# Kernel tuning notes

Measured on AMD Instinct MI355X. Metric: run time of the kernel, lower is better.

The kernel has to match this reference:

```python
import jax, jax.numpy as jnp
import numpy as np

MOLS = 64
ATOMS = 256
N = MOLS * ATOMS
K_GB = 32
K_GNN = 16
HID = 128
OFFSET = 0.009            # GB dielectric offset (nm)
ALPHA, BETA, GAMMA = 1.0, 0.8, 4.85  # OBC2 coefficients
EPS_FACTOR = 138.935456   # Coulomb constant, kJ*nm/(mol*e^2)
PREF = -EPS_FACTOR * (1.0 - 1.0 / 78.5)


def _edges(key, k_neigh):
    # random intra-molecule neighbors, no self loops (mimics radius-graph structure)
    src = jnp.repeat(jnp.arange(N), k_neigh)
    off = jax.random.randint(key, (N * k_neigh,), 1, ATOMS)
    dst = (src // ATOMS) * ATOMS + (src % ATOMS + off) % ATOMS
    return jnp.stack([src, dst]).astype(jnp.int32)


def setup_inputs() -> dict:
    key = jax.random.key(0)
    ks = jax.random.split(key, 8)
    pos = (jax.random.uniform(ks[0], (N, 3), jnp.float32) * 1.5)
    q = jax.random.uniform(ks[1], (N, 1), jnp.float32) - 0.5
    rad = 0.15 + 0.05 * jax.random.uniform(ks[2], (N, 1), jnp.float32)
    scl = 0.8 + 0.2 * jax.random.uniform(ks[3], (N, 1), jnp.float32)
    rest = jax.random.uniform(ks[4], (N, 4), jnp.float32)
    atom_features = jnp.concatenate([q, rad, scl, rest], axis=1)
    batch = jnp.repeat(jnp.arange(MOLS), ATOMS).astype(jnp.int32)
    edge_index = _edges(ks[5], K_GB)
    gnn_edge_index = _edges(ks[6], K_GNN)

    def lin(k, fi, fo):
        return (jax.random.normal(k, (fi, fo), jnp.float32) / np.float32(np.sqrt(fi)),
                jnp.zeros((fo,), jnp.float32))
    kw = jax.random.split(ks[7], 6)
    i1_w1, i1_b1 = lin(kw[0], 2 * 2 + 1, HID)
    i1_w2, i1_b2 = lin(kw[1], HID, HID)
    i2_w1, i2_b1 = lin(kw[2], 2 * HID + 1, HID)
    i2_w2, i2_b2 = lin(kw[3], HID, HID)
    i3_w1, i3_b1 = lin(kw[4], 2 * HID + 1, HID)
    i3_w2, i3_b2 = lin(kw[5], HID, 1)
    return dict(pos=pos, atom_features=atom_features, batch=batch,
                edge_index=edge_index, gnn_edge_index=gnn_edge_index,
                i1_w1=i1_w1, i1_b1=i1_b1, i1_w2=i1_w2, i1_b2=i1_b2,
                i2_w1=i2_w1, i2_b1=i2_b1, i2_w2=i2_w2, i2_b2=i2_b2,
                i3_w1=i3_w1, i3_b1=i3_b1, i3_w2=i3_w2, i3_b2=i3_b2)


def _dist(pos, ei):
    d2 = jnp.sum((pos[ei[0]] - pos[ei[1]]) ** 2, axis=1)
    return jnp.sqrt(d2 + 1e-12)


def _gb_energies(pos, feats, ei):
    # GBNeck_interaction (Born radii via HCT descreening integral, OBC2 rescale)
    # followed by GBNeck_energies (pairwise GB + self energy), per-atom [N,1]
    n = pos.shape[0]
    src, dst = ei[0], ei[1]
    d = _dist(pos, ei)
    q, radius, scale = feats[:, 0], feats[:, 1], feats[:, 2]
    rho = radius - OFFSET
    sr_j = (scale * rho)[src]
    rho_i = rho[dst]
    U = d + sr_j
    L = jnp.maximum(rho_i, jnp.abs(d - sr_j))
    I = 0.5 * (1.0 / L - 1.0 / U
               + 0.25 * (d - sr_j ** 2 / d) * (1.0 / U ** 2 - 1.0 / L ** 2)
               + 0.5 * jnp.log(L / U) / d)
    I = jnp.where(rho_i < U, I, 0.0)
    Isum = jax.ops.segment_sum(I, dst, num_segments=n)
    psi = Isum * rho
    B = 1.0 / (1.0 / rho - jnp.tanh(ALPHA * psi - BETA * psi ** 2 + GAMMA * psi ** 3) / radius)
    Bi, Bj = B[dst], B[src]
    f_gb = jnp.sqrt(d ** 2 + Bi * Bj * jnp.exp(-d ** 2 / (4.0 * Bi * Bj)))
    e_pair = 0.5 * PREF * q[dst] * q[src] / f_gb  # 0.5: edges are double counted
    e = 0.5 * PREF * q ** 2 / B + jax.ops.segment_sum(e_pair, dst, num_segments=n)
    return e[:, None]


def _in_layer(x, ei, d, w1, b1, w2, b2):
    # IN_layer_all_swish_2pass: edge MLP on [x_i || x_j || d] + scatter-add
    n = x.shape[0]
    m = jnp.concatenate([x[ei[0]], x[ei[1]], d[:, None]], axis=1)
    h = jax.nn.silu(m @ w1 + b1)
    return jax.ops.segment_sum(h @ w2 + b2, ei[1], num_segments=n)


def _energies_all(pos, feats, ei, gei,
                  i1_w1, i1_b1, i1_w2, i1_b2,
                  i2_w1, i2_b1, i2_w2, i2_b2,
                  i3_w1, i3_b1, i3_w2, i3_b2):
    e_gb = _gb_energies(pos, feats, ei)
    d_gnn = _dist(pos, gei)
    x = jax.nn.silu(_in_layer(feats[:, :2], gei, d_gnn, i1_w1, i1_b1, i1_w2, i1_b2))
    x = jax.nn.silu(_in_layer(x, gei, d_gnn, i2_w1, i2_b1, i2_w2, i2_b2))
    x = _in_layer(x, gei, d_gnn, i3_w1, i3_b1, i3_w2, i3_b2)
    return e_gb + x


def reference(pos, atom_features, batch, edge_index, gnn_edge_index,
              i1_w1, i1_b1, i1_w2, i1_b2,
              i2_w1, i2_b1, i2_w2, i2_b2,
              i3_w1, i3_b1, i3_w2, i3_b2):
    ws = (i1_w1, i1_b1, i1_w2, i1_b2, i2_w1, i2_b1, i2_w2, i2_b2,
          i3_w1, i3_b1, i3_w2, i3_b2)
    efun = lambda p: _energies_all(p, atom_features, edge_index, gnn_edge_index, *ws)
    energies, vjp = jax.vjp(efun, pos)  # [N,1]
    (gpos,) = vjp(jnp.ones_like(energies))
    forces = -gpos
    energy = jax.ops.segment_sum(energies[:, 0], batch, num_segments=MOLS)[:, None]
    return energy, forces
```

## Files before the change

kernel.cpp:

```cpp
#include <hip/hip_runtime.h>
#include <hip/hip_bf16.h>

#define NATOMS 16384
#define MOLS   64
#define ATOMSM 256
#define EGB    524288
#define EGNN   262144
#define HID    128
#define NH     (NATOMS*HID)

#define OFFSETC 0.009f
#define ALPHAC  1.0f
#define BETAC   0.8f
#define GAMMAC  4.85f
#define PREFC   (-138.935456f*(1.0f-1.0f/78.5f))

typedef __hip_bfloat16 bf;
typedef __attribute__((ext_vector_type(8))) short bf8v;
typedef __attribute__((ext_vector_type(4))) float f4v;

__device__ __forceinline__ float b2f(bf x){ return __bfloat162float(x); }
__device__ __forceinline__ bf f2b(float x){ return __float2bfloat16(x); }
__device__ __forceinline__ short f2s(float x){ bf h = f2b(x); return *(short*)&h; }
__device__ __forceinline__ float s2f(short s){
    unsigned int x = ((unsigned int)(unsigned short)s) << 16;
    return __uint_as_float(x);
}
__device__ __forceinline__ float sigf(float x){ return 1.0f/(1.0f+__expf(-x)); }
__device__ __forceinline__ float waveRed(float v){
    v += __shfl_xor(v,32); v += __shfl_xor(v,16); v += __shfl_xor(v,8);
    v += __shfl_xor(v,4);  v += __shfl_xor(v,2);  v += __shfl_xor(v,1);
    return v;
}

__global__ __launch_bounds__(256) void k_gbA_dist(
    const float* __restrict__ pos, const float* __restrict__ feat,
    const int* __restrict__ ei, float* __restrict__ Isum,
    const int* __restrict__ gei, float* __restrict__ dgnn, int* __restrict__ cnt)
{
    int tid = threadIdx.x;
    if (blockIdx.x < 512){
        __shared__ float sPx[256], sPy[256], sPz[256], sRho[256], sSr[256];
        __shared__ float sI[256];
        int mbase = (blockIdx.x >> 3) * 256;
        {
            int i = mbase + tid;
            sPx[tid]=pos[3*i]; sPy[tid]=pos[3*i+1]; sPz[tid]=pos[3*i+2];
            float rad = feat[7*i+1], sc = feat[7*i+2];
            float rho = rad - OFFSETC;
            sRho[tid]=rho; sSr[tid]=sc*rho;
            sI[tid]=0.f;
        }
        __syncthreads();
        int T = blockIdx.x*256 + tid;
        int s = T >> 3, p = T & 7;
        int sl = s & 255;
        int e0 = s*32 + p*4;
        float px = sPx[sl], py = sPy[sl], pz = sPz[sl];
        float sr = sSr[sl];
        const int* dP = ei + EGB;
#pragma unroll
        for (int j=0;j<4;j++){
            int dl = dP[e0+j] & 255;
            float dx = px - sPx[dl];
            float dy = py - sPy[dl];
            float dz = pz - sPz[dl];
            float d  = sqrtf(dx*dx+dy*dy+dz*dz + 1e-12f);
            float rho_i = sRho[dl];
            float U = d + sr;
            if (rho_i < U){
                float L = fmaxf(rho_i, fabsf(d - sr));
                float invU = 1.0f/U, invL = 1.0f/L;
                float I = 0.5f*invL - 0.5f*invU
                        + 0.125f*(d - sr*sr/d)*(invU*invU - invL*invL)
                        + 0.25f*__logf(L*invU)/d;
                atomicAdd(&sI[dl], I);
            }
        }
        __syncthreads();
        atomicAdd(&Isum[mbase + tid], sI[tid]);
    } else {
        int e = (blockIdx.x-512)*256 + tid;
        if (e >= EGNN) return;
        int s = gei[e], dd = gei[EGNN+e];
        float dx = pos[3*s+0] - pos[3*dd+0];
        float dy = pos[3*s+1] - pos[3*dd+1];
        float dz = pos[3*s+2] - pos[3*dd+2];
        dgnn[e] = sqrtf(dx*dx+dy*dy+dz*dz + 1e-12f);
        atomicAdd(&cnt[dd], 1);
    }
}

__global__ __launch_bounds__(256) void k_gbB_scan(
    const float* __restrict__ feat, const float* __restrict__ Isum,
    float* __restrict__ Bv, float* __restrict__ cB, float* __restrict__ gB,
    float* __restrict__ egb,
    const int* __restrict__ cnt, int* __restrict__ rptr, int* __restrict__ cursor)
{
    int t = threadIdx.x;
    if (blockIdx.x < 64){
        int i = blockIdx.x*256 + t;
        float q   = feat[7*i+0];
        float rad = feat[7*i+1];
        float rho = rad - OFFSETC;
        float psi = Isum[i]*rho;
        float u = psi*(ALPHAC + psi*(-BETAC + GAMMAC*psi));
        float tt = tanhf(u);
        float B = 1.0f/(1.0f/rho - tt/rad);
        Bv[i] = B;
        float du = ALPHAC + psi*(-2.0f*BETAC + 3.0f*GAMMAC*psi);
        cB[i] = B*B*((1.0f-tt*tt)/rad)*du*rho;
        float Cs = 0.5f*PREFC*q*q;
        egb[i] = Cs/B;
        gB[i]  = -Cs/(B*B);
    } else {
        __shared__ int sc[256];
        int m = blockIdx.x - 64;
        int c = cnt[m*256+t];
        sc[t] = c; __syncthreads();
        for (int off=1; off<256; off<<=1){
            int x = (t>=off) ? sc[t-off] : 0;
            __syncthreads();
            sc[t] += x;
            __syncthreads();
        }
        int ex = m*4096 + sc[t] - c;
        rptr[m*256+t] = ex;
        cursor[m*256+t] = ex;
    }
}

__global__ __launch_bounds__(256) void k_gbC(
    const float* __restrict__ pos, const float* __restrict__ feat,
    const int* __restrict__ ei, const float* __restrict__ Bv,
    float* __restrict__ egb, float* __restrict__ gdgb, float* __restrict__ gB)
{
    __shared__ float sPx[256], sPy[256], sPz[256], sB[256], sQf[256];
    __shared__ float sE[256], sG[256];
    int tid = threadIdx.x;
    int mbase = (blockIdx.x >> 3) * 256;
    {
        int i = mbase + tid;
        sPx[tid]=pos[3*i]; sPy[tid]=pos[3*i+1]; sPz[tid]=pos[3*i+2];
        sB[tid]=Bv[i]; sQf[tid]=feat[7*i+0];
        sE[tid]=0.f; sG[tid]=0.f;
    }
    __syncthreads();
    int T = blockIdx.x*256 + tid;
    int s = T >> 3, p = T & 7;
    int sl = s & 255;
    int e0 = s*32 + p*4;
    float px = sPx[sl], py = sPy[sl], pz = sPz[sl];
    float qs = sQf[sl];
    float Bs = sB[sl];
    float gsrc = 0.f;
    const int* dP = ei + EGB;
#pragma unroll
    for (int j=0;j<4;j++){
        int dl = dP[e0+j] & 255;
        float dx = px - sPx[dl];
        float dy = py - sPy[dl];
        float dz = pz - sPz[dl];
        float d2 = dx*dx+dy*dy+dz*dz + 1e-12f;
        float d  = sqrtf(d2);
        float Bd = sB[dl];
        float C = 0.5f*PREFC*sQf[dl]*qs;
        float P = Bd*Bs;
        float ex = __expf(-d2/(4.f*P));
        float f2 = d2 + P*ex;
        float f  = sqrtf(f2);
        float f3i = 1.f/(f2*f);
        gdgb[e0+j] = -C*d*(1.f - 0.25f*ex)*f3i;
        float common = -C*ex*(1.f + d2/(4.f*P))*0.5f*f3i;
        atomicAdd(&sE[dl], C/f);
        atomicAdd(&sG[dl], common*Bs);
        gsrc += common*Bd;
    }
    gsrc += __shfl_xor(gsrc,1);
    gsrc += __shfl_xor(gsrc,2);
    gsrc += __shfl_xor(gsrc,4);
    if (p==0) atomicAdd(&sG[sl], gsrc);
    __syncthreads();
    atomicAdd(&egb[mbase + tid], sE[tid]);
    atomicAdd(&gB[mbase + tid],  sG[tid]);
}

__global__ __launch_bounds__(256) void k_gbE(
    const float* __restrict__ pos, const float* __restrict__ feat,
    const int* __restrict__ ei, const float* __restrict__ cB,
    const float* __restrict__ gB,
    const float* __restrict__ gdgb, float* __restrict__ grad)
{
    __shared__ float sPx[256], sPy[256], sPz[256], sRho[256], sSr[256], sCg[256];
    __shared__ float sGx[256], sGy[256], sGz[256];
    int tid = threadIdx.x;
    int mbase = (blockIdx.x >> 3) * 256;
    {
        int i = mbase + tid;
        sPx[tid]=pos[3*i]; sPy[tid]=pos[3*i+1]; sPz[tid]=pos[3*i+2];
        float rad = feat[7*i+1], sc = feat[7*i+2];
        float rho = rad - OFFSETC;
        sRho[tid]=rho; sSr[tid]=sc*rho;
        sCg[tid]=cB[i]*gB[i];
        sGx[tid]=0.f; sGy[tid]=0.f; sGz[tid]=0.f;
    }
    __syncthreads();
    int T = blockIdx.x*256 + tid;
    int s = T >> 3, p = T & 7;
    int sl = s & 255;
    int e0 = s*32 + p*4;
    float px = sPx[sl], py = sPy[sl], pz = sPz[sl];
    float sr = sSr[sl];
    float gx=0.f, gy=0.f, gz=0.f;
    const int* dP = ei + EGB;
#pragma unroll
    for (int j=0;j<4;j++){
        int dl = dP[e0+j] & 255;
        float dx = px - sPx[dl];
        float dy = py - sPy[dl];
        float dz = pz - sPz[dl];
        float d2 = dx*dx+dy*dy+dz*dz + 1e-12f;
        float d  = sqrtf(d2);
        float rho_i = sRho[dl];
        float U = d + sr;
        float gd = gdgb[e0+j];
        if (rho_i < U){
            float aa = fabsf(d - sr);
            float L, Lp;
            if (rho_i >= aa){ L = rho_i; Lp = 0.f; }
            else { L = aa; Lp = (d >= sr) ? 1.f : -1.f; }
            float invU = 1.f/U, invL = 1.f/L;
            float invU2=invU*invU, invL2=invL*invL;
            float dIdd = -0.5f*Lp*invL2 + 0.5f*invU2
                + 0.125f*(1.f + sr*sr/d2)*(invU2 - invL2)
                + 0.125f*(d - sr*sr/d)*(2.f*Lp*invL2*invL - 2.f*invU2*invU)
                + 0.25f*((Lp*invL - invU)/d - __logf(L*invU)/d2);
            gd += sCg[dl]*dIdd;
        }
        float c = gd/d;
        gx += c*dx; gy += c*dy; gz += c*dz;
        atomicAdd(&sGx[dl], -c*dx);
        atomicAdd(&sGy[dl], -c*dy);
        atomicAdd(&sGz[dl], -c*dz);
    }
    gx += __shfl_xor(gx,1); gx += __shfl_xor(gx,2); gx += __shfl_xor(gx,4);
    gy += __shfl_xor(gy,1); gy += __shfl_xor(gy,2); gy += __shfl_xor(gy,4);
    gz += __shfl_xor(gz,1); gz += __shfl_xor(gz,2); gz += __shfl_xor(gz,4);
    if (p==0){
        atomicAdd(&sGx[sl], gx);
        atomicAdd(&sGy[sl], gy);
        atomicAdd(&sGz[sl], gz);
    }
    __syncthreads();
    int i = mbase + tid;
    atomicAdd(&grad[3*i+0], sGx[tid]);
    atomicAdd(&grad[3*i+1], sGy[tid]);
    atomicAdd(&grad[3*i+2], sGz[tid]);
}

__global__ __launch_bounds__(256) void k_fill(
    const int* __restrict__ gei, int* __restrict__ cursor, int* __restrict__ csr)
{
    int e = blockIdx.x*256 + threadIdx.x;
    if (e >= EGNN) return;
    int dst = gei[EGNN+e];
    int pos = atomicAdd(&cursor[dst], 1);
    csr[pos] = e;
}

__global__ __launch_bounds__(256) void k_pre(
    const float* __restrict__ A2, const float* __restrict__ C1,
    const float* __restrict__ A3, const float* __restrict__ C2,
    short* __restrict__ C1t, short* __restrict__ C2t,
    short* __restrict__ A2at, short* __restrict__ A2bt,
    short* __restrict__ A3at, short* __restrict__ A3bt,
    short* __restrict__ rA2a, short* __restrict__ rA2b,
    short* __restrict__ rA3a, short* __restrict__ rA3b,
    short* __restrict__ rC1, short* __restrict__ rC2,
    const float* __restrict__ feat, const float* __restrict__ A1,
    bf* __restrict__ u1, bf* __restrict__ v1)
{
    if (blockIdx.x < 64){
        int gid = blockIdx.x*256 + threadIdx.x;
        int j = gid >> 7, k = gid & 127;
        C1t[gid]  = f2s(C1[k*HID+j]);
        C2t[gid]  = f2s(C2[k*HID+j]);
        A2at[gid] = f2s(A2[k*HID+j]);
        A2bt[gid] = f2s(A2[(HID+k)*HID+j]);
        A3at[gid] = f2s(A3[k*HID+j]);
        A3bt[gid] = f2s(A3[(HID+k)*HID+j]);
        rA2a[gid] = f2s(A2[gid]);
        rA2b[gid] = f2s(A2[HID*HID+gid]);
        rA3a[gid] = f2s(A3[gid]);
        rA3b[gid] = f2s(A3[HID*HID+gid]);
        rC1[gid]  = f2s(C1[gid]);
        rC2[gid]  = f2s(C2[gid]);
    } else {
        int gid = (blockIdx.x-64)*256 + threadIdx.x;
        int i = gid >> 7, k = gid & 127;
        float q = feat[7*i+0], r = feat[7*i+1];
        u1[gid] = f2b(q*A1[k]       + r*A1[HID+k]);
        v1[gid] = f2b(q*A1[2*HID+k] + r*A1[3*HID+k]);
    }
}

__global__ __launch_bounds__(128) void k_edge_fwd_dst(
    const int* __restrict__ csr, const int* __restrict__ rptr, const int* __restrict__ cnt,
    const float* __restrict__ dgnn, const bf* __restrict__ u, const bf* __restrict__ v,
    const float* __restrict__ wdp, const float* __restrict__ bb,
    bf* __restrict__ Hs, bf* __restrict__ Sds)
{
    int dst = blockIdx.x, k = threadIdx.x;
    int n = cnt[dst], r0 = rptr[dst];
    float wd = wdp[k];
    float base = b2f(v[dst*HID+k]) + bb[k];
    float hsum = 0.f, dssum = 0.f;
    const short* us = (const short*)u;
#pragma unroll 2
    for (int j=0;j<n;j++){
        int e = csr[r0+j];
        float a = s2f(us[(size_t)(e>>4)*HID + k]) + base + dgnn[e]*wd;
        float sg = sigf(a);
        hsum += a*sg;
        dssum += sg*(1.f + a*(1.f - sg));
    }
    Hs[dst*HID+k] = f2b(hsum);
    Sds[dst*HID+k] = f2b(dssum);
}

__global__ __launch_bounds__(256) void k_node_fwd_uv_mfma(
    const short* __restrict__ Hs, const int* __restrict__ cnt,
    const short* __restrict__ Ct, const float* __restrict__ D,
    const short* __restrict__ Aat, const short* __restrict__ Abt,
    bf* __restrict__ dsz, bf* __restrict__ u, bf* __restrict__ v)
{
    __shared__ short sx[64*HID];
    int lane = threadIdx.x & 63, w = threadIdx.x >> 6;
    int m0 = blockIdx.x*64 + w*16;
    int ar = lane & 15, kg = lane >> 4;
    bf8v af[4];
#pragma unroll
    for (int s=0;s<4;s++) af[s] = *(const bf8v*)&Hs[(size_t)(m0+ar)*HID + s*32 + kg*8];
    f4v acc[8];
#pragma unroll
    for (int nt=0;nt<8;nt++){
        acc[nt] = (f4v){0.f,0.f,0.f,0.f};
        const short* bp = Ct + (nt*16+ar)*HID + kg*8;
#pragma unroll
        for (int s=0;s<4;s++){
            bf8v bv = *(const bf8v*)(bp + s*32);
            acc[nt] = __builtin_amdgcn_mfma_f32_16x16x32_bf16(af[s], bv, acc[nt], 0,0,0);
        }
    }
    float cn[4];
#pragma unroll
    for (int r=0;r<4;r++) cn[r] = (float)cnt[m0 + kg*4 + r];
#pragma unroll
    for (int nt=0;nt<8;nt++){
        int j = nt*16 + ar;
        float Dj = D[j];
#pragma unroll
        for (int r=0;r<4;r++){
            int m = m0 + kg*4 + r;
            float zv = acc[nt][r] + cn[r]*Dj;
            float sg = sigf(zv);
// ... 60 lines not shown
#pragma unroll
        for (int s=0;s<4;s++)
            ad_[s] = *(const bf8v*)&Gd[(size_t)(m0+ar)*HID + s*32 + kg*8];
    }
    f4v acc[8];
#pragma unroll
    for (int nt=0;nt<8;nt++){
        acc[nt] = (f4v){0.f,0.f,0.f,0.f};
        const short* bpa = Ra + (nt*16+ar)*HID + kg*8;
        const short* bpb = Rb + (nt*16+ar)*HID + kg*8;
#pragma unroll
        for (int s=0;s<4;s++){
            bf8v ba = *(const bf8v*)(bpa + s*32);
            bf8v bb = *(const bf8v*)(bpb + s*32);
            acc[nt] = __builtin_amdgcn_mfma_f32_16x16x32_bf16(as_[s], ba, acc[nt], 0,0,0);
            acc[nt] = __builtin_amdgcn_mfma_f32_16x16x32_bf16(ad_[s], bb, acc[nt], 0,0,0);
        }
    }
#pragma unroll
    for (int nt=0;nt<8;nt++){
        int j = nt*16 + ar;
#pragma unroll
        for (int r=0;r<4;r++){
            int m = m0 + kg*4 + r;
            float t = acc[nt][r] * b2f(dsz[(size_t)m*HID + j]);
            st[(w*16 + kg*4 + r)*HID + j] = f2s(t);
        }
    }
    __syncthreads();
    bf8v af[4];
#pragma unroll
    for (int s=0;s<4;s++) af[s] = *(const bf8v*)&st[(w*16+ar)*HID + s*32 + kg*8];
    f4v a2[8];
#pragma unroll
    for (int nt=0;nt<8;nt++){
        a2[nt] = (f4v){0.f,0.f,0.f,0.f};
        const short* bp = Rc + (nt*16+ar)*HID + kg*8;
#pragma unroll
        for (int s=0;s<4;s++){
            bf8v bc = *(const bf8v*)(bp + s*32);
            a2[nt] = __builtin_amdgcn_mfma_f32_16x16x32_bf16(af[s], bc, a2[nt], 0,0,0);
        }
    }
#pragma unroll
    for (int nt=0;nt<8;nt++){
        int j = nt*16 + ar;
#pragma unroll
        for (int r=0;r<4;r++){
            gHout[(size_t)(m0 + kg*4 + r)*HID + j] = f2b(a2[nt][r]);
        }
    }
}

__global__ __launch_bounds__(128) void k_l3_dst(
    const int* __restrict__ csr, const int* __restrict__ rptr, const int* __restrict__ cnt,
    const float* __restrict__ dgnn, const bf* __restrict__ u, const bf* __restrict__ v,
    const float* __restrict__ A3, const float* __restrict__ B3,
    const float* __restrict__ C3, const float* __restrict__ D3,
    bf* __restrict__ Gd, float* __restrict__ x3)
{
    __shared__ float rr[2];
    int dst = blockIdx.x, k = threadIdx.x;
    int n = cnt[dst], r0 = rptr[dst];
    float wd = A3[256*HID+k], ck = C3[k];
    float base = b2f(v[dst*HID+k]) + B3[k];
    float hsum = 0.f, dssum = 0.f;
    const short* us = (const short*)u;
#pragma unroll 2
    for (int j=0;j<n;j++){
        int e = csr[r0+j];
        float a = s2f(us[(size_t)(e>>4)*HID + k]) + base + dgnn[e]*wd;
        float sg = sigf(a);
        hsum += a*sg;
        dssum += sg*(1.f + a*(1.f - sg));
    }
    Gd[dst*HID+k] = f2b(ck*dssum);
    float pv = waveRed(ck*hsum);
    if ((k&63)==0) rr[k>>6] = pv;
    __syncthreads();
    if (k==0) x3[dst] = rr[0] + rr[1] + (float)n*D3[0];
}

__global__ __launch_bounds__(128) void k_l3_src(
    const int* __restrict__ gei, const float* __restrict__ dgnn,
    const bf* __restrict__ u, const bf* __restrict__ v,
    const float* __restrict__ A3, const float* __restrict__ B3,
    const float* __restrict__ C3,
    bf* __restrict__ Gs, float* __restrict__ gdg)
{
    __shared__ short sv[2048];
    __shared__ float sQ[16][130];
    int s = blockIdx.x, k = threadIdx.x;
    {
        int t = k >> 3, q = k & 7;
        int dst = gei[EGNN + s*16 + t];
        const bf8v* vr = (const bf8v*)((const short*)v + (size_t)dst*HID);
        ((bf8v*)sv)[t*16 + q*2]     = vr[q*2];
        ((bf8v*)sv)[t*16 + q*2 + 1] = vr[q*2+1];
    }
    __syncthreads();
    float uk = b2f(u[s*HID+k]);
    float wd = A3[256*HID+k], bk = B3[k], ck = C3[k];
    float cw = ck*wd;
    float gs = 0.f;
    const float* dgp = dgnn + s*16;
#pragma unroll
    for (int t=0;t<16;t++){
        float a = uk + s2f(sv[t*128+k]) + dgp[t]*wd + bk;
        float sg = sigf(a);
        float dv = sg*(1.f + a*(1.f - sg));
        gs += dv;
        sQ[t][k] = dv*cw;
    }
    Gs[s*HID+k] = f2b(ck*gs);
    __syncthreads();
    int t = k >> 3, r = k & 7;
    float pg = 0.f;
#pragma unroll
    for (int i=0;i<16;i++) pg += sQ[t][i + 16*r];
    pg += __shfl_xor(pg,1); pg += __shfl_xor(pg,2); pg += __shfl_xor(pg,4);
    if (r==0) gdg[s*16+t] = pg;
}

__global__ __launch_bounds__(128) void k_bwd_src(
    const int* __restrict__ gei, const float* __restrict__ dgnn,
    const bf* __restrict__ u, const bf* __restrict__ v,
    const float* __restrict__ wdp, const float* __restrict__ bb,
    const bf* __restrict__ gH,
    bf* __restrict__ Gs, float* __restrict__ gdg)
{
    __shared__ short sv[2048];
    __shared__ short sgh[2048];
    __shared__ float sQ[16][130];
    int s = blockIdx.x, k = threadIdx.x;
    {
        int t = k >> 3, q = k & 7;
        int dst = gei[EGNN + s*16 + t];
        const bf8v* vr = (const bf8v*)((const short*)v + (size_t)dst*HID);
        const bf8v* gr = (const bf8v*)((const short*)gH + (size_t)dst*HID);
        ((bf8v*)sv)[t*16 + q*2]      = vr[q*2];
        ((bf8v*)sv)[t*16 + q*2 + 1]  = vr[q*2+1];
        ((bf8v*)sgh)[t*16 + q*2]     = gr[q*2];
        ((bf8v*)sgh)[t*16 + q*2 + 1] = gr[q*2+1];
    }
    __syncthreads();
    float uk = b2f(u[s*HID+k]);
    float wd = wdp[k], bk = bb[k];
    float gs = 0.f;
    const float* dgp = dgnn + s*16;
#pragma unroll
    for (int t=0;t<16;t++){
        float a = uk + s2f(sv[t*128+k]) + dgp[t]*wd + bk;
        float sg = sigf(a);
        float dv = sg*(1.f + a*(1.f - sg));
        float ga = s2f(sgh[t*128+k]) * dv;
        gs += ga;
        sQ[t][k] = ga*wd;
    }
    Gs[s*HID+k] = f2b(gs);
    __syncthreads();
    int t = k >> 3, r = k & 7;
    float pg = 0.f;
#pragma unroll
    for (int i=0;i<16;i++) pg += sQ[t][i + 16*r];
    pg += __shfl_xor(pg,1); pg += __shfl_xor(pg,2); pg += __shfl_xor(pg,4);
    if (r==0) gdg[s*16+t] += pg;
}

__global__ __launch_bounds__(128) void k_bwd1_src(
    const int* __restrict__ gei, const float* __restrict__ dgnn,
    const bf* __restrict__ u, const bf* __restrict__ v,
    const float* __restrict__ wdp, const float* __restrict__ bb,
    const bf* __restrict__ gH, float* __restrict__ gdg)
{
    __shared__ short sv[2048];
    __shared__ short sgh[2048];
    __shared__ float sQ[16][130];
    int s = blockIdx.x, k = threadIdx.x;
    {
        int t = k >> 3, q = k & 7;
        int dst = gei[EGNN + s*16 + t];
        const bf8v* vr = (const bf8v*)((const short*)v + (size_t)dst*HID);
        const bf8v* gr = (const bf8v*)((const short*)gH + (size_t)dst*HID);
        ((bf8v*)sv)[t*16 + q*2]      = vr[q*2];
        ((bf8v*)sv)[t*16 + q*2 + 1]  = vr[q*2+1];
        ((bf8v*)sgh)[t*16 + q*2]     = gr[q*2];
        ((bf8v*)sgh)[t*16 + q*2 + 1] = gr[q*2+1];
    }
    __syncthreads();
    float uk = b2f(u[s*HID+k]);
    float wd = wdp[k], bk = bb[k];
    const float* dgp = dgnn + s*16;
#pragma unroll
    for (int t=0;t<16;t++){
        float a = uk + s2f(sv[t*128+k]) + dgp[t]*wd + bk;
        float sg = sigf(a);
        float dv = sg*(1.f + a*(1.f - sg));
        sQ[t][k] = s2f(sgh[t*128+k]) * dv * wd;
    }
    __syncthreads();
    int t = k >> 3, r = k & 7;
    float pg = 0.f;
#pragma unroll
    for (int i=0;i<16;i++) pg += sQ[t][i + 16*r];
    pg += __shfl_xor(pg,1); pg += __shfl_xor(pg,2); pg += __shfl_xor(pg,4);
    if (r==0) gdg[s*16+t] += pg;
}

__global__ __launch_bounds__(256) void k_force_atom(
    const float* __restrict__ pos, const int* __restrict__ gei,
    const int* __restrict__ csr, const int* __restrict__ rptr, const int* __restrict__ cnt,
    const float* __restrict__ dgnn, const float* __restrict__ gdg,
    const float* __restrict__ grad, float* __restrict__ fout)
{
    int T = blockIdx.x*256 + threadIdx.x;
    int i = T >> 3, p = T & 7;
    float px = pos[3*i+0], py = pos[3*i+1], pz = pos[3*i+2];
    float ax=0.f, ay=0.f, az=0.f;
    for (int j=p;j<16;j+=8){
        int e = i*16 + j;
        int o = gei[EGNN+e];
        float c = gdg[e]/dgnn[e];
        ax += c*(px - pos[3*o+0]);
        ay += c*(py - pos[3*o+1]);
        az += c*(pz - pos[3*o+2]);
    }
    int n = cnt[i], r0 = rptr[i];
    for (int j=p;j<n;j+=8){
        int e = csr[r0+j];
        int o = e >> 4;
        float c = gdg[e]/dgnn[e];
        ax += c*(px - pos[3*o+0]);
        ay += c*(py - pos[3*o+1]);
        az += c*(pz - pos[3*o+2]);
    }
    ax += __shfl_xor(ax,1); ax += __shfl_xor(ax,2); ax += __shfl_xor(ax,4);
    ay += __shfl_xor(ay,1); ay += __shfl_xor(ay,2); ay += __shfl_xor(ay,4);
    az += __shfl_xor(az,1); az += __shfl_xor(az,2); az += __shfl_xor(az,4);
    if (p==0){
        fout[3*i+0] = -(grad[3*i+0] + ax);
        fout[3*i+1] = -(grad[3*i+1] + ay);
        fout[3*i+2] = -(grad[3*i+2] + az);
    }
}

__global__ __launch_bounds__(256) void k_final(
    const float* __restrict__ egb, const float* __restrict__ x3,
    float* __restrict__ out)
{
    __shared__ float red[4];
    int m = blockIdx.x, tid = threadIdx.x;
    int i = m*ATOMSM + tid;
    float en = egb[i] + x3[i];
    float v = waveRed(en);
    int wave = tid>>6, lane = tid&63;
    if (lane==0) red[wave] = v;
    __syncthreads();
    if (tid==0) out[m] = red[0]+red[1]+red[2]+red[3];
}

extern "C" void kernel_launch(void* const* d_in, const int* in_sizes, int n_in,
                              void* d_out, int out_size, void* d_ws, size_t ws_size,
                              hipStream_t stream)
{
    const float* pos  = (const float*)d_in[0];
    const float* feat = (const float*)d_in[1];
    const int* ei  = (const int*)d_in[3];
    const int* gei = (const int*)d_in[4];
    const float* A1f = (const float*)d_in[5];  const float* B1f = (const float*)d_in[6];
    const float* C1f = (const float*)d_in[7];  const float* D1f = (const float*)d_in[8];
    const float* A2f = (const float*)d_in[9];  const float* B2f = (const float*)d_in[10];
    const float* C2f = (const float*)d_in[11]; const float* D2f = (const float*)d_in[12];
    const float* A3f = (const float*)d_in[13]; const float* B3f = (const float*)d_in[14];
    const float* C3f = (const float*)d_in[15]; const float* D3f = (const float*)d_in[16];

    float* w = (float*)d_ws;
    size_t off = 0;
    auto nxt = [&](size_t n)->float*{ float* p = w + off; off += (n + 255) & ~(size_t)255; return p; };
    float* Isum = nxt(NATOMS);
    int*   cnt  = (int*)nxt(NATOMS);
    float* grad = nxt(3*NATOMS);
    float* Bv = nxt(NATOMS); float* cB = nxt(NATOMS);
    float* gB = nxt(NATOMS); float* egb = nxt(NATOMS); float* x3 = nxt(NATOMS);
    int*   rptr = (int*)nxt(NATOMS);
    int*   curs = (int*)nxt(NATOMS);
    int*   csr  = (int*)nxt(EGNN);
    float* dgnn = nxt(EGNN); float* gdgnn = nxt(EGNN); float* gdgb = nxt(EGB);
    bf* dsz1 = (bf*)nxt(NH/2); bf* dsz2 = (bf*)nxt(NH/2);
    bf* Hs1 = (bf*)nxt(NH/2); bf* Hs2 = (bf*)nxt(NH/2);
    bf* Gs3 = (bf*)nxt(NH/2); bf* Gd3 = (bf*)nxt(NH/2);
    bf* Sds2 = (bf*)nxt(NH/2);
    bf* u1 = (bf*)nxt(NH/2); bf* v1 = (bf*)nxt(NH/2);
    bf* u2 = (bf*)nxt(NH/2); bf* v2 = (bf*)nxt(NH/2);
    bf* u3 = (bf*)nxt(NH/2); bf* v3 = (bf*)nxt(NH/2);
    short* C1t  = (short*)nxt(8192); short* C2t  = (short*)nxt(8192);
    short* A2at = (short*)nxt(8192); short* A2bt = (short*)nxt(8192);
    short* A3at = (short*)nxt(8192); short* A3bt = (short*)nxt(8192);
    short* rA2a = (short*)nxt(8192); short* rA2b = (short*)nxt(8192);
    short* rA3a = (short*)nxt(8192); short* rA3b = (short*)nxt(8192);
    short* rC1  = (short*)nxt(8192); short* rC2  = (short*)nxt(8192);
    bf* gH2 = Hs2;
    bf* Gs2 = Gs3;
    bf* gH1 = Hs1;

    hipMemsetAsync(Isum, 0, (size_t)5*NATOMS*sizeof(float), stream);

    k_pre<<<64+NH/256,256,0,stream>>>(A2f, C1f, A3f, C2f,
        C1t, C2t, A2at, A2bt, A3at, A3bt, rA2a, rA2b, rA3a, rA3b, rC1, rC2,
        feat, A1f, u1, v1);

    k_gbA_dist<<<512+EGNN/256,256,0,stream>>>(pos, feat, ei, Isum, gei, dgnn, cnt);
    k_gbB_scan<<<128,256,0,stream>>>(feat, Isum, Bv, cB, gB, egb, cnt, rptr, curs);
    k_fill<<<EGNN/256,256,0,stream>>>(gei, curs, csr);
    k_gbC<<<512,256,0,stream>>>(pos, feat, ei, Bv, egb, gdgb, gB);
    k_gbE<<<512,256,0,stream>>>(pos, feat, ei, cB, gB, gdgb, grad);

    k_edge_fwd_dst<<<NATOMS,128,0,stream>>>(csr, rptr, cnt, dgnn, u1, v1,
                                            A1f+4*HID, B1f, Hs1, Sds2 );
    k_node_fwd_uv_mfma<<<NATOMS/64,256,0,stream>>>((const short*)Hs1, cnt, C1t, D1f,
                                                   A2at, A2bt, dsz1, u2, v2);
    k_edge_fwd_dst<<<NATOMS,128,0,stream>>>(csr, rptr, cnt, dgnn, u2, v2,
                                            A2f+256*HID, B2f, Hs2, Sds2);
    k_node_fwd_uv_mfma<<<NATOMS/64,256,0,stream>>>((const short*)Hs2, cnt, C2t, D2f,
                                                   A3at, A3bt, dsz2, u3, v3);

    k_l3_dst<<<NATOMS,128,0,stream>>>(csr, rptr, cnt, dgnn, u3, v3,
                                      A3f, B3f, C3f, D3f, Gd3, x3);
    k_l3_src<<<NATOMS,128,0,stream>>>(gei, dgnn, u3, v3, A3f, B3f, C3f, Gs3, gdgnn);

    k_gx_node_bwd_mfma<<<NATOMS/64,256,0,stream>>>((const short*)Gs3, (const short*)Gd3,
        (const short*)nullptr, (const short*)nullptr, rA3a, rA3b, dsz2, rC2, gH2);
    k_bwd_src<<<NATOMS,128,0,stream>>>(gei, dgnn, u2, v2, A2f+256*HID, B2f, gH2,
                                       Gs2, gdgnn);
    k_gx_node_bwd_mfma<<<NATOMS/64,256,0,stream>>>((const short*)Gs2, (const short*)nullptr,
        (const short*)gH2, (const short*)Sds2, rA2a, rA2b, dsz1, rC1, gH1);
    k_bwd1_src<<<NATOMS,128,0,stream>>>(gei, dgnn, u1, v1, A1f+4*HID, B1f, gH1, gdgnn);

    k_force_atom<<<NATOMS*8/256,256,0,stream>>>(pos, gei, csr, rptr, cnt, dgnn, gdgnn,
                                                grad, (float*)d_out + MOLS);
    k_final<<<MOLS,256,0,stream>>>(egb, x3, (float*)d_out);
}
```

Baseline: 386.4 us.

## Merge independent kernels into shared launches and halve per-thread GB edge work

Several independent kernels now share a launch by splitting on block index: GB C with the CSR fill, GB E with the first edge-forward layer, layer-3 dst with layer-3 src, and the force gather with the final energy reduction. This removes launch gaps and lets independent work overlap on the device. The GB passes also switch from 8 to 16 threads per source atom with 2 edges each, doubling the block count, and edge_fwd_dst packs two destination atoms per 256-thread block. In exchange, fused blocks with different branches share one register and LDS footprint, and the finer GB split adds more shared-memory atomics per edge.

New measurement: 390.1 us. Within noise of the previous version (+1.0%).

```diff
diff --git a/kernel.cpp b/kernel.cpp
--- a/kernel.cpp
+++ b/kernel.cpp
@@ -32,6 +32,11 @@
     v += __shfl_xor(v,4);  v += __shfl_xor(v,2);  v += __shfl_xor(v,1);
     return v;
 }
+__device__ __forceinline__ float red16(float v){
+    v += __shfl_xor(v,1); v += __shfl_xor(v,2);
+    v += __shfl_xor(v,4); v += __shfl_xor(v,8);
+    return v;
+}
 
 __global__ __launch_bounds__(256) void k_gbA_dist(
     const float* __restrict__ pos, const float* __restrict__ feat,
@@ -39,10 +44,10 @@
     const int* __restrict__ gei, float* __restrict__ dgnn, int* __restrict__ cnt)
 {
     int tid = threadIdx.x;
-    if (blockIdx.x < 512){
+    if (blockIdx.x < 1024){
         __shared__ float sPx[256], sPy[256], sPz[256], sRho[256], sSr[256];
         __shared__ float sI[256];
-        int mbase = (blockIdx.x >> 3) * 256;
+        int mbase = (blockIdx.x >> 4) * 256;
         {
             int i = mbase + tid;
             sPx[tid]=pos[3*i]; sPy[tid]=pos[3*i+1]; sPz[tid]=pos[3*i+2];
@@ -53,14 +58,14 @@
         }
         __syncthreads();
         int T = blockIdx.x*256 + tid;
-        int s = T >> 3, p = T & 7;
+        int s = T >> 4, p = T & 15;
         int sl = s & 255;
-        int e0 = s*32 + p*4;
+        int e0 = s*32 + p*2;
         float px = sPx[sl], py = sPy[sl], pz = sPz[sl];
         float sr = sSr[sl];
         const int* dP = ei + EGB;
 #pragma unroll
-        for (int j=0;j<4;j++){
+        for (int j=0;j<2;j++){
             int dl = dP[e0+j] & 255;
             float dx = px - sPx[dl];
             float dy = py - sPy[dl];
@@ -80,7 +85,7 @@
         __syncthreads();
         atomicAdd(&Isum[mbase + tid], sI[tid]);
     } else {
-        int e = (blockIdx.x-512)*256 + tid;
+        int e = (blockIdx.x-1024)*256 + tid;
         if (e >= EGNN) return;
         int s = gei[e], dd = gei[EGNN+e];
         float dx = pos[3*s+0] - pos[3*dd+0];
@@ -130,142 +135,161 @@
     }
 }
 
-__global__ __launch_bounds__(256) void k_gbC(
+__global__ __launch_bounds__(256) void k_gbC_fill(
     const float* __restrict__ pos, const float* __restrict__ feat,
     const int* __restrict__ ei, const float* __restrict__ Bv,
-    float* __restrict__ egb, float* __restrict__ gdgb, float* __restrict__ gB)
-{
-    __shared__ float sPx[256], sPy[256], sPz[256], sB[256], sQf[256];
-    __shared__ float sE[256], sG[256];
+    float* __restrict__ egb, float* __restrict__ gdgb, float* __restrict__ gB,
+    const int* __restrict__ gei, int* __restrict__ cursor, int* __restrict__ csr)
+{
     int tid = threadIdx.x;
-    int mbase = (blockIdx.x >> 3) * 256;
-    {
-        int i = mbase + tid;
-        sPx[tid]=pos[3*i]; sPy[tid]=pos[3*i+1]; sPz[tid]=pos[3*i+2];
-        sB[tid]=Bv[i]; sQf[tid]=feat[7*i+0];
-        sE[tid]=0.f; sG[tid]=0.f;
-    }
-    __syncthreads();
-    int T = blockIdx.x*256 + tid;
-    int s = T >> 3, p = T & 7;
-    int sl = s & 255;
-    int e0 = s*32 + p*4;
-    float px = sPx[sl], py = sPy[sl], pz = sPz[sl];
-    float qs = sQf[sl];
-    float Bs = sB[sl];
-    float gsrc = 0.f;
-    const int* dP = ei + EGB;
-#pragma unroll
-    for (int j=0;j<4;j++){
-        int dl = dP[e0+j] & 255;
-        float dx = px - sPx[dl];
-        float dy = py - sPy[dl];
-        float dz = pz - sPz[dl];
-        float d2 = dx*dx+dy*dy+dz*dz + 1e-12f;
-        float d  = sqrtf(d2);
-        float Bd = sB[dl];
-        float C = 0.5f*PREFC*sQf[dl]*qs;
-        float P = Bd*Bs;
-        float ex = __expf(-d2/(4.f*P));
-        float f2 = d2 + P*ex;
-        float f  = sqrtf(f2);
-        float f3i = 1.f/(f2*f);
-        gdgb[e0+j] = -C*d*(1.f - 0.25f*ex)*f3i;
-        float common = -C*ex*(1.f + d2/(4.f*P))*0.5f*f3i;
-        atomicAdd(&sE[dl], C/f);
-        atomicAdd(&sG[dl], common*Bs);
-        gsrc += common*Bd;
-    }
-    gsrc += __shfl_xor(gsrc,1);
-    gsrc += __shfl_xor(gsrc,2);
-    gsrc += __shfl_xor(gsrc,4);
-    if (p==0) atomicAdd(&sG[sl], gsrc);
-    __syncthreads();
-    atomicAdd(&egb[mbase + tid], sE[tid]);
-    atomicAdd(&gB[mbase + tid],  sG[tid]);
-}
-
-__global__ __launch_bounds__(256) void k_gbE(
+    if (blockIdx.x < 1024){
+        __shared__ float sPx[256], sPy[256], sPz[256], sB[256], sQf[256];
+        __shared__ float sE[256], sG[256];
+        int mbase = (blockIdx.x >> 4) * 256;
+        {
+            int i = mbase + tid;
+            sPx[tid]=pos[3*i]; sPy[tid]=pos[3*i+1]; sPz[tid]=pos[3*i+2];
+            sB[tid]=Bv[i]; sQf[tid]=feat[7*i+0];
+            sE[tid]=0.f; sG[tid]=0.f;
+        }
+        __syncthreads();
+        int T = blockIdx.x*256 + tid;
+        int s = T >> 4, p = T & 15;
+        int sl = s & 255;
+        int e0 = s*32 + p*2;
+        float px = sPx[sl], py = sPy[sl], pz = sPz[sl];
+        float qs = sQf[sl];
+        float Bs = sB[sl];
+        float gsrc = 0.f;
+        const int* dP = ei + EGB;
+#pragma unroll
+        for (int j=0;j<2;j++){
+            int dl = dP[e0+j] & 255;
+            float dx = px - sPx[dl];
+            float dy = py - sPy[dl];
+            float dz = pz - sPz[dl];
+            float d2 = dx*dx+dy*dy+dz*dz + 1e-12f;
+            float d  = sqrtf(d2);
+            float Bd = sB[dl];
+            float C = 0.5f*PREFC*sQf[dl]*qs;
+            float P = Bd*Bs;
+            float ex = __expf(-d2/(4.f*P));
+            float f2 = d2 + P*ex;
+            float f  = sqrtf(f2);
+            float f3i = 1.f/(f2*f);
+            gdgb[e0+j] = -C*d*(1.f - 0.25f*ex)*f3i;
+            float common = -C*ex*(1.f + d2/(4.f*P))*0.5f*f3i;
+            atomicAdd(&sE[dl], C/f);
+            atomicAdd(&sG[dl], common*Bs);
+            gsrc += common*Bd;
+        }
+        gsrc = red16(gsrc);
+        if (p==0) atomicAdd(&sG[sl], gsrc);
+        __syncthreads();
+        atomicAdd(&egb[mbase + tid], sE[tid]);
+        atomicAdd(&gB[mbase + tid],  sG[tid]);
+    } else {
+        int e = (blockIdx.x-1024)*256 + tid;
+        if (e >= EGNN) return;
+        int dst = gei[EGNN+e];
+        int posn = atomicAdd(&cursor[dst], 1);
+        csr[posn] = e;
+    }
+}
+
+__global__ __launch_bounds__(256) void k_gbE_fwd1(
     const float* __restrict__ pos, const float* __restrict__ feat,
     const int* __restrict__ ei, const float* __restrict__ cB,
     const float* __restrict__ gB,
-    const float* __restrict__ gdgb, float* __restrict__ grad)
-{
-    __shared__ float sPx[256], sPy[256], sPz[256], sRho[256], sSr[256], sCg[256];
-    __shared__ float sGx[256], sGy[256], sGz[256];
+    const float* __restrict__ gdgb, float* __restrict__ grad,
+    const int* __restrict__ csr, const int* __restrict__ rptr, const int* __restrict__ cnt,
+    const float* __restrict__ dgnn, const bf* __restrict__ u, const bf* __restrict__ v,
+    const float* __restrict__ wdp, const float* __restrict__ bb,
+    bf* __restrict__ Hs, bf* __restrict__ Sds)
+{
     int tid = threadIdx.x;
-    int mbase = (blockIdx.x >> 3) * 256;
-    {
+    if (blockIdx.x < 1024){
+        __shared__ float sPx[256], sPy[256], sPz[256], sRho[256], sSr[256], sCg[256];
+        __shared__ float sGx[256], sGy[256], sGz[256];
+        int mbase = (blockIdx.x >> 4) * 256;
+        {
+            int i = mbase + tid;
+            sPx[tid]=pos[3*i]; sPy[tid]=pos[3*i+1]; sPz[tid]=pos[3*i+2];
+            float rad = feat[7*i+1], sc = feat[7*i+2];
+            float rho = rad - OFFSETC;
+            sRho[tid]=rho; sSr[tid]=sc*rho;
+            sCg[tid]=cB[i]*gB[i];
+            sGx[tid]=0.f; sGy[tid]=0.f; sGz[tid]=0.f;
+        }
+        __syncthreads();
+        int T = blockIdx.x*256 + tid;
+        int s = T >> 4, p = T & 15;
+        int sl = s & 255;
+        int e0 = s*32 + p*2;
+        float px = sPx[sl], py = sPy[sl], pz = sPz[sl];
+        float sr = sSr[sl];
+        float gx=0.f, gy=0.f, gz=0.f;
+        const int* dP = ei + EGB;
+#pragma unroll
+        for (int j=0;j<2;j++){
+            int dl = dP[e0+j] & 255;
+            float dx = px - sPx[dl];
+            float dy = py - sPy[dl];
+            float dz = pz - sPz[dl];
+            float d2 = dx*dx+dy*dy+dz*dz + 1e-12f;
+            float d  = sqrtf(d2);
+            float rho_i = sRho[dl];
+            float U = d + sr;
+            float gd = gdgb[e0+j];
+            if (rho_i < U){
+                float aa = fabsf(d - sr);
+                float L, Lp;
+                if (rho_i >= aa){ L = rho_i; Lp = 0.f; }
+                else { L = aa; Lp = (d >= sr) ? 1.f : -1.f; }
+                float invU = 1.f/U, invL = 1.f/L;
+                float invU2=invU*invU, invL2=invL*invL;
+                float dIdd = -0.5f*Lp*invL2 + 0.5f*invU2
+                    + 0.125f*(1.f + sr*sr/d2)*(invU2 - invL2)
+                    + 0.125f*(d - sr*sr/d)*(2.f*Lp*invL2*invL - 2.f*invU2*invU)
+                    + 0.25f*((Lp*invL - invU)/d - __logf(L*invU)/d2);
+                gd += sCg[dl]*dIdd;
+            }
+            float c = gd/d;
+            gx += c*dx; gy += c*dy; gz += c*dz;
+            atomicAdd(&sGx[dl], -c*dx);
+            atomicAdd(&sGy[dl], -c*dy);
+            atomicAdd(&sGz[dl], -c*dz);
+        }
+        gx = red16(gx); gy = red16(gy); gz = red16(gz);
+        if (p==0){
+            atomicAdd(&sGx[sl], gx);
+            atomicAdd(&sGy[sl], gy);
+            atomicAdd(&sGz[sl], gz);
+        }
+        __syncthreads();
         int i = mbase + tid;
-        sPx[tid]=pos[3*i]; sPy[tid]=pos[3*i+1]; sPz[tid]=pos[3*i+2];
-        float rad = feat[7*i+1], sc = feat[7*i+2];
-        float rho = rad - OFFSETC;
-        sRho[tid]=rho; sSr[tid]=sc*rho;
-        sCg[tid]=cB[i]*gB[i];
-        sGx[tid]=0.f; sGy[tid]=0.f; sGz[tid]=0.f;
-    }
-    __syncthreads();
-    int T = blockIdx.x*256 + tid;
-    int s = T >> 3, p = T & 7;
-    int sl = s & 255;
-    int e0 = s*32 + p*4;
-    float px = sPx[sl], py = sPy[sl], pz = sPz[sl];
-    float sr = sSr[sl];
-    float gx=0.f, gy=0.f, gz=0.f;
-    const int* dP = ei + EGB;
-#pragma unroll
-    for (int j=0;j<4;j++){
-        int dl = dP[e0+j] & 255;
-        float dx = px - sPx[dl];
-        float dy = py - sPy[dl];
-        float dz = pz - sPz[dl];
-        float d2 = dx*dx+dy*dy+dz*dz + 1e-12f;
-        float d  = sqrtf(d2);
-        float rho_i = sRho[dl];
-        float U = d + sr;
-        float gd = gdgb[e0+j];
-        if (rho_i < U){
-            float aa = fabsf(d - sr);
-            float L, Lp;
-            if (rho_i >= aa){ L = rho_i; Lp = 0.f; }
-            else { L = aa; Lp = (d >= sr) ? 1.f : -1.f; }
-            float invU = 1.f/U, invL = 1.f/L;
-            float invU2=invU*invU, invL2=invL*invL;
-            float dIdd = -0.5f*Lp*invL2 + 0.5f*invU2
-                + 0.125f*(1.f + sr*sr/d2)*(invU2 - invL2)
-                + 0.125f*(d - sr*sr/d)*(2.f*Lp*invL2*invL - 2.f*invU2*invU)
-                + 0.25f*((Lp*invL - invU)/d - __logf(L*invU)/d2);
-            gd += sCg[dl]*dIdd;
-        }
-        float c = gd/d;
-        gx += c*dx; gy += c*dy; gz += c*dz;
-        atomicAdd(&sGx[dl], -c*dx);
-        atomicAdd(&sGy[dl], -c*dy);
-        atomicAdd(&sGz[dl], -c*dz);
-    }
-    gx += __shfl_xor(gx,1); gx += __shfl_xor(gx,2); gx += __shfl_xor(gx,4);
-    gy += __shfl_xor(gy,1); gy += __shfl_xor(gy,2); gy += __shfl_xor(gy,4);
-    gz += __shfl_xor(gz,1); gz += __shfl_xor(gz,2); gz += __shfl_xor(gz,4);
-    if (p==0){
-        atomicAdd(&sGx[sl], gx);
-        atomicAdd(&sGy[sl], gy);
-        atomicAdd(&sGz[sl], gz);
-    }
-    __syncthreads();
-    int i = mbase + tid;
-    atomicAdd(&grad[3*i+0], sGx[tid]);
-    atomicAdd(&grad[3*i+1], sGy[tid]);
-    atomicAdd(&grad[3*i+2], sGz[tid]);
-}
-
-__global__ __launch_bounds__(256) void k_fill(
-    const int* __restrict__ gei, int* __restrict__ cursor, int* __restrict__ csr)
-{
-    int e = blockIdx.x*256 + threadIdx.x;
-    if (e >= EGNN) return;
-    int dst = gei[EGNN+e];
-    int pos = atomicAdd(&cursor[dst], 1);
-    csr[pos] = e;
+        atomicAdd(&grad[3*i+0], sGx[tid]);
+        atomicAdd(&grad[3*i+1], sGy[tid]);
+        atomicAdd(&grad[3*i+2], sGz[tid]);
+    } else {
+        int dst = (blockIdx.x-1024)*2 + (tid>>7);
+        int k = tid & 127;
+        int n = cnt[dst], r0 = rptr[dst];
+        float wd = wdp[k];
+        float base = b2f(v[dst*HID+k]) + bb[k];
+        float hsum = 0.f, dssum = 0.f;
+        const short* us = (const short*)u;
+#pragma unroll 2
+        for (int j=0;j<n;j++){
+            int e = csr[r0+j];
+            float a = s2f(us[(size_t)(e>>4)*HID + k]) + base + dgnn[e]*wd;
+            float sg = sigf(a);
+            hsum += a*sg;
+            dssum += sg*(1.f + a*(1.f - sg));
+        }
+        Hs[dst*HID+k] = f2b(hsum);
+        Sds[dst*HID+k] = f2b(dssum);
+    }
 }
 
 __global__ __launch_bounds__(256) void k_pre(
@@ -304,13 +328,14 @@
     }
 }
 
-__global__ __launch_bounds__(128) void k_edge_fwd_dst(
+__global__ __launch_bounds__(256) void k_edge_fwd_dst(
     const int* __restrict__ csr, const int* __restrict__ rptr, const int* __restrict__ cnt,
     const float* __restrict__ dgnn, const bf* __restrict__ u, const bf* __restrict__ v,
     const float* __restrict__ wdp, const float* __restrict__ bb,
     bf* __restrict__ Hs, bf* __restrict__ Sds)
 {
-    int dst = blockIdx.x, k = threadIdx.x;
+    int dst = blockIdx.x*2 + (threadIdx.x>>7);
+    int k = threadIdx.x & 127;
     int n = cnt[dst], r0 = rptr[dst];
     float wd = wdp[k];
     float base = b2f(v[dst*HID+k]) + bb[k];
@@ -477,74 +502,71 @@
     }
 }
 
-__global__ __launch_bounds__(128) void k_l3_dst(
+__global__ __launch_bounds__(128) void k_l3(
+    const int* __restrict__ gei,
     const int* __restrict__ csr, const int* __restrict__ rptr, const int* __restrict__ cnt,
     const float* __restrict__ dgnn, const bf* __restrict__ u, const bf* __restrict__ v,
     const float* __restrict__ A3, const float* __restrict__ B3,
     const float* __restrict__ C3, const float* __restrict__ D3,
-    bf* __restrict__ Gd, float* __restrict__ x3)
-{
-    __shared__ float rr[2];
-    int dst = blockIdx.x, k = threadIdx.x;
-    int n = cnt[dst], r0 = rptr[dst];
-    float wd = A3[256*HID+k], ck = C3[k];
-    float base = b2f(v[dst*HID+k]) + B3[k];
-    float hsum = 0.f, dssum = 0.f;
-    const short* us = (const short*)u;
+    bf* __restrict__ Gd, float* __restrict__ x3,
+    bf* __restrict__ Gs, float* __restrict__ gdg)
+{
+    int k = threadIdx.x;
+    if (blockIdx.x < NATOMS){
+        __shared__ float rr[2];
+        int dst = blockIdx.x;
+        int n = cnt[dst], r0 = rptr[dst];
+        float wd = A3[256*HID+k], ck = C3[k];
+        float base = b2f(v[dst*HID+k]) + B3[k];
+        float hsum = 0.f, dssum = 0.f;
+        const short* us = (const short*)u;
 #pragma unroll 2
-    for (int j=0;j<n;j++){
-        int e = csr[r0+j];
-        float a = s2f(us[(size_t)(e>>4)*HID + k]) + base + dgnn[e]*wd;
-        float sg = sigf(a);
-        hsum += a*sg;
-        dssum += sg*(1.f + a*(1.f - sg));
-    }
-    Gd[dst*HID+k] = f2b(ck*dssum);
-    float pv = waveRed(ck*hsum);
-    if ((k&63)==0) rr[k>>6] = pv;
-    __syncthreads();
-    if (k==0) x3[dst] = rr[0] + rr[1] + (float)n*D3[0];
-}
-
-__global__ __launch_bounds__(128) void k_l3_src(
-    const int* __restrict__ gei, const float* __restrict__ dgnn,
-    const bf* __restrict__ u, const bf* __restrict__ v,
-    const float* __restrict__ A3, const float* __restrict__ B3,
-    const float* __restrict__ C3,
-    bf* __restrict__ Gs, float* __restrict__ gdg)
-{
-    __shared__ short sv[2048];
-    __shared__ float sQ[16][130];
-    int s = blockIdx.x, k = threadIdx.x;
-    {
-        int t = k >> 3, q = k & 7;
-        int dst = gei[EGNN + s*16 + t];
-        const bf8v* vr = (const bf8v*)((const short*)v + (size_t)dst*HID);
-        ((bf8v*)sv)[t*16 + q*2]     = vr[q*2];
-        ((bf8v*)sv)[t*16 + q*2 + 1] = vr[q*2+1];
-    }
-    __syncthreads();
-    float uk = b2f(u[s*HID+k]);
-    float wd = A3[256*HID+k], bk = B3[k], ck = C3[k];
-    float cw = ck*wd;
-    float gs = 0.f;
-    const float* dgp = dgnn + s*16;
-#pragma unroll
-    for (int t=0;t<16;t++){
-        float a = uk + s2f(sv[t*128+k]) + dgp[t]*wd + bk;
-        float sg = sigf(a);
-        float dv = sg*(1.f + a*(1.f - sg));
-        gs += dv;
-        sQ[t][k] = dv*cw;
-    }
-    Gs[s*HID+k] = f2b(ck*gs);
-    __syncthreads();
-    int t = k >> 3, r = k & 7;
-    float pg = 0.f;
-#pragma unroll
-    for (int i=0;i<16;i++) pg += sQ[t][i + 16*r];
-    pg += __shfl_xor(pg,1); pg += __shfl_xor(pg,2); pg += __shfl_xor(pg,4);
-    if (r==0) gdg[s*16+t] = pg;
+        for (int j=0;j<n;j++){
+            int e = csr[r0+j];
+            float a = s2f(us[(size_t)(e>>4)*HID + k]) + base + dgnn[e]*wd;
+            float sg = sigf(a);
+            hsum += a*sg;
+            dssum += sg*(1.f + a*(1.f - sg));
+        }
+        Gd[dst*HID+k] = f2b(ck*dssum);
+        float pv = waveRed(ck*hsum);
+        if ((k&63)==0) rr[k>>6] = pv;
+        __syncthreads();
+        if (k==0) x3[dst] = rr[0] + rr[1] + (float)n*D3[0];
+    } else {
+        __shared__ short sv[2048];
+        __shared__ float sQ[16][130];
+        int s = blockIdx.x - NATOMS;
+        {
+            int t = k >> 3, q = k & 7;
+            int dst = gei[EGNN + s*16 + t];
+            const bf8v* vr = (const bf8v*)((const short*)v + (size_t)dst*HID);
+            ((bf8v*)sv)[t*16 + q*2]     = vr[q*2];
+            ((bf8v*)sv)[t*16 + q*2 + 1] = vr[q*2+1];
+        }
+        __syncthreads();
+        float uk = b2f(u[s*HID+k]);
+        float wd = A3[256*HID+k], bk = B3[k], ck = C3[k];
+        float cw = ck*wd;
+        float gs = 0.f;
+        const float* dgp = dgnn + s*16;
+#pragma unroll
+        for (int t=0;t<16;t++){
+            float a = uk + s2f(sv[t*128+k]) + dgp[t]*wd + bk;
+            float sg = sigf(a);
+            float dv = sg*(1.f + a*(1.f - sg));
+            gs += dv;
+            sQ[t][k] = dv*cw;
+        }
+        Gs[s*HID+k] = f2b(ck*gs);
+        __syncthreads();
+        int t = k >> 3, r = k & 7;
+        float pg = 0.f;
+#pragma unroll
+        for (int i=0;i<16;i++) pg += sQ[t][i + 16*r];
+        pg += __shfl_xor(pg,1); pg += __shfl_xor(pg,2); pg += __shfl_xor(pg,4);
+        if (r==0) gdg[s*16+t] = pg;
+    }
 }
 
 __global__ __launch_bounds__(128) void k_bwd_src(
@@ -632,56 +654,57 @@
     if (r==0) gdg[s*16+t] += pg;
 }
 
-__global__ __launch_bounds__(256) void k_force_atom(
+__global__ __launch_bounds__(256) void k_force_final(
     const float* __restrict__ pos, const int* __restrict__ gei,
     const int* __restrict__ csr, const int* __restrict__ rptr, const int* __restrict__ cnt,
     const float* __restrict__ dgnn, const float* __restrict__ gdg,
-    const float* __restrict__ grad, float* __restrict__ fout)
-{
-    int T = blockIdx.x*256 + threadIdx.x;
-    int i = T >> 3, p = T & 7;
-    float px = pos[3*i+0], py = pos[3*i+1], pz = pos[3*i+2];
-    float ax=0.f, ay=0.f, az=0.f;
-    for (int j=p;j<16;j+=8){
-        int e = i*16 + j;
-        int o = gei[EGNN+e];
-        float c = gdg[e]/dgnn[e];
-        ax += c*(px - pos[3*o+0]);
-        ay += c*(py - pos[3*o+1]);
-        az += c*(pz - pos[3*o+2]);
-    }
-    int n = cnt[i], r0 = rptr[i];
-    for (int j=p;j<n;j+=8){
-        int e = csr[r0+j];
-        int o = e >> 4;
-        float c = gdg[e]/dgnn[e];
-        ax += c*(px - pos[3*o+0]);
-        ay += c*(py - pos[3*o+1]);
-        az += c*(pz - pos[3*o+2]);
-    }
-    ax += __shfl_xor(ax,1); ax += __shfl_xor(ax,2); ax += __shfl_xor(ax,4);
-    ay += __shfl_xor(ay,1); ay += __shfl_xor(ay,2); ay += __shfl_xor(ay,4);
-    az += __shfl_xor(az,1); az += __shfl_xor(az,2); az += __shfl_xor(az,4);
-    if (p==0){
-        fout[3*i+0] = -(grad[3*i+0] + ax);
-        fout[3*i+1] = -(grad[3*i+1] + ay);
-        fout[3*i+2] = -(grad[3*i+2] + az);
-    }
-}
-
-__global__ __launch_bounds__(256) void k_final(
+    const float* __restrict__ grad,
     const float* __restrict__ egb, const float* __restrict__ x3,
     float* __restrict__ out)
 {
-    __shared__ float red[4];
-    int m = blockIdx.x, tid = threadIdx.x;
-    int i = m*ATOMSM + tid;
-    float en = egb[i] + x3[i];
-    float v = waveRed(en);
-    int wave = tid>>6, lane = tid&63;
-    if (lane==0) red[wave] = v;
-    __syncthreads();
-    if (tid==0) out[m] = red[0]+red[1]+red[2]+red[3];
+    int tid = threadIdx.x;
+    if (blockIdx.x < 512){
+        float* fout = out + MOLS;
+        int T = blockIdx.x*256 + tid;
+        int i = T >> 3, p = T & 7;
+        float px = pos[3*i+0], py = pos[3*i+1], pz = pos[3*i+2];
+        float ax=0.f, ay=0.f, az=0.f;
+        for (int j=p;j<16;j+=8){
+            int e = i*16 + j;
+            int o = gei[EGNN+e];
+            float c = gdg[e]/dgnn[e];
+            ax += c*(px - pos[3*o+0]);
+            ay += c*(py - pos[3*o+1]);
+            az += c*(pz - pos[3*o+2]);
+        }
+        int n = cnt[i], r0 = rptr[i];
+        for (int j=p;j<n;j+=8){
+            int e = csr[r0+j];
+            int o = e >> 4;
+            float c = gdg[e]/dgnn[e];
+            ax += c*(px - pos[3*o+0]);
+            ay += c*(py - pos[3*o+1]);
+            az += c*(pz - pos[3*o+2]);
+        }
+        ax += __shfl_xor(ax,1); ax += __shfl_xor(ax,2); ax += __shfl_xor(ax,4);
+        ay += __shfl_xor(ay,1); ay += __shfl_xor(ay,2); ay += __shfl_xor(ay,4);
+        az += __shfl_xor(az,1); az += __shfl_xor(az,2); az += __shfl_xor(az,4);
+        if (p==0){
+            fout[3*i+0] = -(grad[3*i+0] + ax);
+            fout[3*i+1] = -(grad[3*i+1] + ay);
+            fout[3*i+2] = -(grad[3*i+2] + az);
+        }
+    } else {
+        __shared__ float red[4];
+        int m = blockIdx.x - 512;
+        int i = m*ATOMSM + tid;
+        float en = egb[i] + x3[i];
+        float vv = waveRed(en);
+        int wave = tid>>6, lane = tid&63;
+        if (lane==0) red[wave] = vv;
+        __syncthreads();
+        if (tid==0) out[m] = red[0]+red[1]+red[2]+red[3];
+    }
 }
 
 extern "C" void kernel_launch(void* const* d_in, const int* in_sizes, int n_in,
@@ -734,24 +757,23 @@
         C1t, C2t, A2at, A2bt, A3at, A3bt, rA2a, rA2b, rA3a, rA3b, rC1, rC2,
         feat, A1f, u1, v1);
 
-    k_gbA_dist<<<512+EGNN/256,256,0,stream>>>(pos, feat, ei, Isum, gei, dgnn, cnt);
+    k_gbA_dist<<<1024+EGNN/256,256,0,stream>>>(pos, feat, ei, Isum, gei, dgnn, cnt);
     k_gbB_scan<<<128,256,0,stream>>>(feat, Isum, Bv, cB, gB, egb, cnt, rptr, curs);
-    k_fill<<<EGNN/256,256,0,stream>>>(gei, curs, csr);
-    k_gbC<<<512,256,0,stream>>>(pos, feat, ei, Bv, egb, gdgb, gB);
-    k_gbE<<<512,256,0,stream>>>(pos, feat, ei, cB, gB, gdgb, grad);
-
-    k_edge_fwd_dst<<<NATOMS,128,0,stream>>>(csr, rptr, cnt, dgnn, u1, v1,
-                                            A1f+4*HID, B1f, Hs1, Sds2 );
+    k_gbC_fill<<<1024+EGNN/256,256,0,stream>>>(pos, feat, ei, Bv, egb, gdgb, gB,
+                                               gei, curs, csr);
+    k_gbE_fwd1<<<1024+NATOMS/2,256,0,stream>>>(pos, feat, ei, cB, gB, gdgb, grad,
+                                               csr, rptr, cnt, dgnn, u1, v1,
+                                               A1f+4*HID, B1f, Hs1, Sds2 );
+
     k_node_fwd_uv_mfma<<<NATOMS/64,256,0,stream>>>((const short*)Hs1, cnt, C1t, D1f,
                                                    A2at, A2bt, dsz1, u2, v2);
-    k_edge_fwd_dst<<<NATOMS,128,0,stream>>>(csr, rptr, cnt, dgnn, u2, v2,
-                                            A2f+256*HID, B2f, Hs2, Sds2);
+    k_edge_fwd_dst<<<NATOMS/2,256,0,stream>>>(csr, rptr, cnt, dgnn, u2, v2,
+                                              A2f+256*HID, B2f, Hs2, Sds2);
     k_node_fwd_uv_mfma<<<NATOMS/64,256,0,stream>>>((const short*)Hs2, cnt, C2t, D2f,
                                                    A3at, A3bt, dsz2, u3, v3);
 
-    k_l3_dst<<<NATOMS,128,0,stream>>>(csr, rptr, cnt, dgnn, u3, v3,
-                                      A3f, B3f, C3f, D3f, Gd3, x3);
-    k_l3_src<<<NATOMS,128,0,stream>>>(gei, dgnn, u3, v3, A3f, B3f, C3f, Gs3, gdgnn);
+    k_l3<<<2*NATOMS,128,0,stream>>>(gei, csr, rptr, cnt, dgnn, u3, v3,
+                                    A3f, B3f, C3f, D3f, Gd3, x3, Gs3, gdgnn);
 
     k_gx_node_bwd_mfma<<<NATOMS/64,256,0,stream>>>((const short*)Gs3, (const short*)Gd3,
         (const short*)nullptr, (const short*)nullptr, rA3a, rA3b, dsz2, rC2, gH2);
@@ -761,7 +783,6 @@
         (const short*)gH2, (const short*)Sds2, rA2a, rA2b, dsz1, rC1, gH1);
     k_bwd1_src<<<NATOMS,128,0,stream>>>(gei, dgnn, u1, v1, A1f+4*HID, B1f, gH1, gdgnn);
 
-    k_force_atom<<<NATOMS*8/256,256,0,stream>>>(pos, gei, csr, rptr, cnt, dgnn, gdgnn,
-                                                grad, (float*)d_out + MOLS);
-    k_final<<<MOLS,256,0,stream>>>(egb, x3, (float*)d_out);
-}
+    k_force_final<<<512+MOLS,256,0,stream>>>(pos, gei, csr, rptr, cnt, dgnn, gdgnn,
+                                             grad, egb, x3, (float*)d_out);
+}
```
